# Optimization experiments

Hardware: AMD Instinct MI355X
Metric: run time of the kernel (lower is better)

The kernel has to match this reference:

```python
import jax, jax.numpy as jnp
import numpy as np

B, T, C = 4, 1024, 1024  # batch, tokens, channel (== head `size`)
H = 8                    # num_heads


def setup_inputs() -> dict:
    key = jax.random.key(0)
    kd, kq, kk, kv = jax.random.split(key, 4)
    data = jax.random.normal(kd, (B, T, C), dtype=jnp.float32)
    # torch nn.Linear(size,size,bias=False) weight is [out,in]; one per head, stacked on axis 0
    s = 1.0 / np.sqrt(C)
    Wq = jax.random.uniform(kq, (H, C, C), dtype=jnp.float32, minval=-s, maxval=s)
    Wk = jax.random.uniform(kk, (H, C, C), dtype=jnp.float32, minval=-s, maxval=s)
    Wv = jax.random.uniform(kv, (H, C, C), dtype=jnp.float32, minval=-s, maxval=s)
    return {"data": data, "Wq": Wq, "Wk": Wk, "Wv": Wv}


def reference(data, Wq, Wk, Wv):
    # per-head projections: y = x @ W.T  -> [B,H,T,C]
    q = jnp.einsum('btc,hdc->bhtd', data, Wq)
    k = jnp.einsum('btc,hdc->bhtd', data, Wk)
    v = jnp.einsum('btc,hdc->bhtd', data, Wv)
    scale = 1.0 / jnp.sqrt(jnp.asarray(C, dtype=data.dtype))
    scores = jnp.einsum('bhtd,bhsd->bhts', q, k) * scale  # [B,H,T,T]
    causal = jnp.tril(jnp.ones((T, T), dtype=bool))
    scores = jnp.where(causal, scores, -jnp.inf)
    w = jax.nn.softmax(scores, axis=-1)
    out = jnp.einsum('bhts,bhsd->bhtd', w, v)            # [B,H,T,C]
    # torch.cat over heads on last dim == [B,T,H,C] reshape to [B,T,H*C]
    return out.transpose(0, 2, 1, 3).reshape(B, T, H * C)
```

## Files before the change

### kernel.cpp

```cpp
#include <hip/hip_runtime.h>
#include <hip/hip_fp16.h>


typedef unsigned short u16;
typedef _Float16 f16x8 __attribute__((ext_vector_type(8)));
typedef float f32x4 __attribute__((ext_vector_type(4)));

__device__ __forceinline__ u16 f2h(float f) {
    union { __half h; u16 u; } cv;
    cv.h = __float2half(f);
    return cv.u;
}
__device__ __forceinline__ float h2f(u16 u) {
    union { __half h; u16 u; } cv;
    cv.u = u;
    return __half2float(cv.h);
}

__device__ __forceinline__ void gload_lds16(const u16* g, const u16* lds_base, unsigned off_bytes) {
    unsigned a32 = (unsigned)(uintptr_t)((const char*)lds_base + off_bytes);
    a32 = __builtin_amdgcn_readfirstlane(a32);
    __builtin_amdgcn_global_load_lds(
        (const __attribute__((address_space(1))) void*)(uintptr_t)g,
        (__attribute__((address_space(3))) void*)a32,
        16, 0, 0);
}

#define M_A 0
#define M_B 1
#define M_C 2
#define M_PV 3

template <int MODE>
__global__ __launch_bounds__(512, 2) void mega(
    const u16* __restrict__ dataH, const u16* __restrict__ WvH,
    const u16* __restrict__ WqT, const u16* __restrict__ WkT,
    u16* __restrict__ MTp, u16* __restrict__ Qp, u16* __restrict__ VTa,
    u16* __restrict__ S16, u16* __restrict__ P16,
    float* __restrict__ outF)
{
    const int C = 1024, T = 1024, HC = 8192;
    const int nb = (MODE == M_A ? 192 : MODE == M_B ? 512 :
                    MODE == M_C ? 768 : 256);
    const int chunk = nb >> 3;
    const int phys = blockIdx.x;
    const int o = (phys & 7) * chunk + (phys >> 3);

    __shared__ u16 lds[8 * 8192];

    const int t = threadIdx.x, w = t >> 6, l = t & 63;
    const int wm = w >> 2, wn = w & 3;
    const int frow = l & 15, fch = l >> 4;
    const int clin = w * 64 + l;
    const int srow = clin >> 2;
    const int sch = (clin & 3) ^ ((clin >> 3) & 3);

    const int NPASS = (MODE == M_PV) ? 2 : 1;

    for (int pass = 0; pass < NPASS; ++pass) {
        const u16 *Ab, *Bb;
        int lda, ldb, ldc, NT, tile_m, tile_n;
        float scale = 1.0f;
        u16* out16 = nullptr;
        float* out32 = nullptr;

        int vfill = -1;
        if (MODE == M_A && o >= 128) vfill = o - 128;
        if (MODE == M_C && o >= 320) vfill = o - 320 + 64;

        if (vfill >= 0) {
            const int vz = vfill >> 4, rem = vfill & 15;
            tile_n = rem & 3; tile_m = rem >> 2;
            Ab = WvH + (size_t)(vz & 7) * C * C + (size_t)tile_m * 256 * C;
            Bb = dataH + (size_t)(vz >> 3) * T * C + (size_t)tile_n * 256 * C;
            lda = C; ldb = C; ldc = T;
            out16 = VTa + (size_t)vz * C * T;
            NT = 16;
        } else if (MODE == M_A) {
            const int h = o >> 4, r = o & 15;
            tile_m = r >> 2; tile_n = r & 3;
            Ab = WkT + (size_t)h * C * C + (size_t)tile_m * 256 * C;
            Bb = WqT + (size_t)h * C * C + (size_t)tile_n * 256 * C;
            lda = C; ldb = C; ldc = C;
            out16 = MTp + (size_t)h * C * C;
            NT = 16;
        } else if (MODE == M_B) {
            const int s = o >> 6, ww = o & 63;
            tile_n = (s & 3) * 8 + (ww & 7);
            tile_m = (s >> 2) * 8 + (ww >> 3);
            Ab = dataH + (size_t)tile_m * 256 * C;
            Bb = MTp + (size_t)(tile_n >> 2) * C * C + (size_t)(tile_n & 3) * 256 * C;
            lda = C; ldb = C; ldc = HC;
            out16 = Qp;
            NT = 16;
        } else if (MODE == M_C) {
            const int qz = o / 10, j = o - qz * 10;
            tile_m = (j >= 1) + (j >= 3) + (j >= 6);
            tile_n = j - (tile_m == 0 ? 0 : tile_m == 1 ? 1 : tile_m == 2 ? 3 : 6);
            Ab = Qp + (size_t)(qz >> 3) * T * HC + (size_t)(qz & 7) * C
                    + (size_t)tile_m * 256 * HC;
            Bb = dataH + (size_t)(qz >> 3) * T * C + (size_t)tile_n * 256 * C;
            lda = HC; ldb = C; ldc = T;
            out16 = S16 + (size_t)qz * T * T;
            scale = 1.0f / 32.0f;
            NT = 16;
        } else {
            const int pz = o >> 3, j = o & 7, x = j & 3, hi = j >> 2;
            tile_m = (pass == 0) ? (hi ? 2 : 3) : (hi ? 1 : 0);
            tile_n = x;
            Ab = P16 + (size_t)pz * T * T + (size_t)tile_m * 256 * T;
            Bb = VTa + (size_t)pz * C * T + (size_t)tile_n * 256 * T;
            lda = T; ldb = T; ldc = HC;
            out32 = outF + (size_t)(pz >> 3) * T * HC + (size_t)(pz & 7) * C;
            NT = (tile_m + 1) * 4;
        }

        if (MODE == M_PV) {
            const int pz = o >> 3;
            const int Kend = NT * 64;
            const u16* Sb = S16 + (size_t)pz * T * T + (size_t)tile_m * 256 * T;
            u16* Pb = P16 + (size_t)pz * T * T + (size_t)tile_m * 256 * T;
            for (int rr = w; rr < 256; rr += 8) {
                const int nrow = tile_m * 256 + rr + 1;
                const u16* rp = Sb + (size_t)rr * T;
                float ev[16];
#pragma unroll
                for (int j = 0; j < 4; ++j) {
                    const int col = j * 256 + l * 4;
                    if (col < Kend) {
                        ushort4 v4 = *(const ushort4*)(rp + col);
                        ev[j * 4 + 0] = (col + 0 < nrow) ? h2f(v4.x) : -3.0e38f;
                        ev[j * 4 + 1] = (col + 1 < nrow) ? h2f(v4.y) : -3.0e38f;
                        ev[j * 4 + 2] = (col + 2 < nrow) ? h2f(v4.z) : -3.0e38f;
                        ev[j * 4 + 3] = (col + 3 < nrow) ? h2f(v4.w) : -3.0e38f;
                    } else {
                        ev[j * 4 + 0] = -3.0e38f; ev[j * 4 + 1] = -3.0e38f;
                        ev[j * 4 + 2] = -3.0e38f; ev[j * 4 + 3] = -3.0e38f;
                    }
                }
                float mx = -3.0e38f;
#pragma unroll
                for (int e = 0; e < 16; ++e) mx = fmaxf(mx, ev[e]);
#pragma unroll
                for (int od = 1; od < 64; od <<= 1) mx = fmaxf(mx, __shfl_xor(mx, od));
                float sum = 0.f;
#pragma unroll
                for (int e = 0; e < 16; ++e) { ev[e] = __expf(ev[e] - mx); sum += ev[e]; }
#pragma unroll
                for (int od = 1; od < 64; od <<= 1) sum += __shfl_xor(sum, od);
                const float inv = 1.0f / sum;
#pragma unroll
                for (int j = 0; j < 4; ++j) {
                    const int col = j * 256 + l * 4;
                    if (col < Kend) {
                        ushort4 o4;
                        o4.x = f2h(ev[j * 4 + 0] * inv);
                        o4.y = f2h(ev[j * 4 + 1] * inv);
                        o4.z = f2h(ev[j * 4 + 2] * inv);
                        o4.w = f2h(ev[j * 4 + 3] * inv);
                        *(ushort4*)(Pb + (size_t)rr * T + col) = o4;
                    }
                }
            }
            asm volatile("s_waitcnt vmcnt(0)");
            __builtin_amdgcn_sched_barrier(0);
            __builtin_amdgcn_s_barrier();
        }

        const long eA = (long)srow * lda + sch * 8;
        const long eB = (long)srow * ldb + sch * 8;

        f32x4 acc[8][4] = {};
        f16x8 af[4], bf[4];

#define STAGE(DB, MAT, KS, TT) do {                                            \
        const u16* g_ = (MAT == 0 ? Ab + (size_t)(TT) * 64 + (KS) * 32 + eA    \
                                  : Bb + (size_t)(TT) * 64 + (KS) * 32 + eB);  \
        const u16* hb_ = lds + ((((DB) << 2) | ((MAT) << 1) | (KS)) << 13);    \
        gload_lds16(g_, hb_, (unsigned)(w * 64 * 16));                         \
        gload_lds16(g_ + (size_t)128 * (MAT == 0 ? lda : ldb), hb_,            \
                    (unsigned)((512 + w * 64) * 16));                          \
    } while (0)

#define RD(DB, MAT, KS, ROW)                                                   \
    (*(const f16x8*)((const char*)(lds + ((((DB) << 2) | ((MAT) << 1) | (KS)) << 13)) + \
                     ((unsigned)((ROW) * 64 + fch * 16) ^ ((((ROW) >> 1) & 3) << 4))))

#define VM6 do { asm volatile("s_waitcnt vmcnt(6)"); \
                 __builtin_amdgcn_sched_barrier(0); } while (0)
#define VM0 do { asm volatile("s_waitcnt vmcnt(0)"); \
                 __builtin_amdgcn_sched_barrier(0); } while (0)
#define NOPW ((void)0)

#define PH(DB, KS, MH, WAITC, ...) do {                                        \
        if ((MH) == 0) {                                                       \
            _Pragma("unroll") for (int ni = 0; ni < 4; ++ni)                   \
                bf[ni] = RD(DB, 1, KS, wn * 64 + ni * 16 + frow);              \
        }                                                                      \
        _Pragma("unroll") for (int m4 = 0; m4 < 4; ++m4)                       \
            af[m4] = RD(DB, 0, KS, wm * 128 + ((MH) * 4 + m4) * 16 + frow);    \
        __VA_ARGS__;                                                           \
        __builtin_amdgcn_sched_barrier(0);                                     \
        __builtin_amdgcn_s_barrier();                                          \
        asm volatile("s_waitcnt lgkmcnt(0)");                                  \
        __builtin_amdgcn_sched_barrier(0);                                     \
        __builtin_amdgcn_s_setprio(1);                                         \
        _Pragma("unroll") for (int m4 = 0; m4 < 4; ++m4)                       \
            _Pragma("unroll") for (int ni = 0; ni < 4; ++ni)                   \
                acc[(MH) * 4 + m4][ni] = __builtin_amdgcn_mfma_f32_16x16x32_f16( \
                    af[m4], bf[ni], acc[(MH) * 4 + m4][ni], 0, 0, 0);          \
        __builtin_amdgcn_s_setprio(0);                                         \
        __builtin_amdgcn_sched_barrier(0);                                     \
        WAITC;                                                                 \
        __builtin_amdgcn_s_barrier();                                          \
    } while (0)

        STAGE(0, 1, 0, 0); STAGE(0, 0, 0, 0); STAGE(0, 1, 1, 0); STAGE(0, 0, 1, 0);
        STAGE(1, 1, 0, 1); STAGE(1, 0, 0, 1); STAGE(1, 1, 1, 1);
        VM6;
        __builtin_amdgcn_s_barrier();

        for (int tt = 0; tt < NT; tt += 2) {
            const bool more = (tt + 2) < NT;
            PH(0, 0, 0, NOPW, STAGE(1, 0, 1, tt + 1));
            PH(0, 0, 1, NOPW, if (more) STAGE(0, 1, 0, tt + 2));
            PH(0, 1, 0, NOPW, if (more) STAGE(0, 0, 0, tt + 2));
            PH(0, 1, 1, if (more) VM6; else VM0,
                        if (more) STAGE(0, 1, 1, tt + 2));
            PH(1, 0, 0, NOPW, if (more) STAGE(0, 0, 1, tt + 2));
            PH(1, 0, 1, NOPW, if (more) STAGE(1, 1, 0, tt + 3));
            PH(1, 1, 0, NOPW, if (more) STAGE(1, 0, 0, tt + 3));
            PH(1, 1, 1, if (more) VM6; else VM0,
                        if (more) STAGE(1, 1, 1, tt + 3));
        }
#undef PH
#undef RD
#undef STAGE
#undef VM6
#undef VM0
#undef NOPW

        const int r0 = (l >> 4) * 4, cc = l & 15;
#pragma unroll
        for (int mi = 0; mi < 8; ++mi) {
#pragma unroll
            for (int r = 0; r < 4; ++r) {
                size_t grow = (size_t)(tile_m * 256 + wm * 128 + mi * 16 + r0 + r);
#pragma unroll
                for (int ni = 0; ni < 4; ++ni) {
                    int gcol = tile_n * 256 + wn * 64 + ni * 16 + cc;
                    float v = acc[mi][ni][r] * scale;
                    if (MODE == M_PV)
                        out32[grow * ldc + gcol] = v;
                    else
                        out16[grow * ldc + gcol] = f2h(v);
                }
            }
        }
    }
}

__global__ __launch_bounds__(256) void cast_setup(
    const float* __restrict__ data, const float* __restrict__ Wq,
    const float* __restrict__ Wk, const float* __restrict__ Wv,
    u16* __restrict__ dataH, u16* __restrict__ WqT,
    u16* __restrict__ WkT, u16* __restrict__ WvH)
{
    const int z = blockIdx.z, tx = threadIdx.x, ty = threadIdx.y;
    if (z < 16) {
        const int h = z & 7;
        const float* src = ((z >> 3) ? Wk : Wq) + (size_t)h * 1048576;
        u16* dst = ((z >> 3) ? WkT : WqT) + (size_t)h * 1048576;
        const int r0 = blockIdx.y * 32, c0 = blockIdx.x * 32;
        __shared__ float tile[32][33];
        for (int i = ty; i < 32; i += 8)
            tile[i][tx] = src[(size_t)(r0 + i) * 1024 + c0 + tx];
        __syncthreads();
        for (int i = ty; i < 32; i += 8)
            dst[(size_t)(c0 + i) * 1024 + r0 + tx] = f2h(tile[tx][i]);
    } else {
        const int tid = ty * 32 + tx;
        const int bid = blockIdx.y * 32 + blockIdx.x;
        const int reps = (z == 16) ? 4 : 8;
        const float* src = (z == 16) ? data : Wv;
        u16* dst = (z == 16) ? dataH : WvH;
        for (int k2 = 0; k2 < reps; ++k2) {
            int i = (k2 * 1024 + bid) * 256 + tid;
            float4 v = ((const float4*)src)[i];
            ushort4 o4;
            o4.x = f2h(v.x); o4.y = f2h(v.y); o4.z = f2h(v.z); o4.w = f2h(v.w);
            ((ushort4*)dst)[i] = o4;
        }
    }
}

extern "C" void kernel_launch(void* const* d_in, const int* in_sizes, int n_in,
                              void* d_out, int out_size, void* d_ws, size_t ws_size,
                              hipStream_t stream)
{
    (void)in_sizes; (void)n_in; (void)out_size; (void)ws_size;
    const int B = 4, T = 1024, C = 1024, H = 8;
    const int BT = B * T, HC = H * C;

    const float* data = (const float*)d_in[0];
    const float* Wq = (const float*)d_in[1];
    const float* Wk = (const float*)d_in[2];
    const float* Wv = (const float*)d_in[3];
    float* out = (float*)d_out;

    char* p = (char*)d_ws;
    const size_t nData = (size_t)BT * C;
    const size_t nW = (size_t)H * C * C;
    const size_t nAll = (size_t)BT * HC;
    const size_t nS = (size_t)B * H * T * T;
    u16* dataH = (u16*)p; p += nData * 2;
    u16* WvH = (u16*)p; p += nW * 2;
    u16* WqT = (u16*)p; p += nW * 2;
    u16* WkT = (u16*)p; p += nW * 2;
    u16* MTp = (u16*)p; p += nW * 2;
    u16* Qp = (u16*)p; p += nAll * 2;
    u16* VTa = (u16*)p; p += nAll * 2;
    u16* S16 = (u16*)p; p += nS * 2;
    u16* P16 = (u16*)p; p += nS * 2;

    cast_setup<<<dim3(32, 32, 18), dim3(32, 8), 0, stream>>>(
        data, Wq, Wk, Wv, dataH, WqT, WkT, WvH);

    mega<M_A><<<dim3(192), dim3(512), 0, stream>>>(
        dataH, WvH, WqT, WkT, MTp, Qp, VTa, S16, P16, out);

    mega<M_B><<<dim3(512), dim3(512), 0, stream>>>(
        dataH, WvH, WqT, WkT, MTp, Qp, VTa, S16, P16, out);

    mega<M_C><<<dim3(768), dim3(512), 0, stream>>>(
        dataH, WvH, WqT, WkT, MTp, Qp, VTa, S16, P16, out);

    mega<M_PV><<<dim3(256), dim3(512), 0, stream>>>(
        dataH, WvH, WqT, WkT, MTp, Qp, VTa, S16, P16, out);
}
```

Before: 450.5 us.

## Fuse four GEMM phase launches into one persistent kernel with grid barriers

Replaces the four separate mega kernel launches with a single persistent 256-block kernel. The phases are separated by software grid barriers built on atomic counters, which are reset inside the setup kernel. Work is redistributed per phase: the projection, score and V tiles are looped over blocks, and the softmax becomes a row-parallel pass over all rows instead of running inside each PV block. The goal is to remove launch gaps and kernel tail effects. The costs are spin-wait barriers and a reliance on all 256 blocks being co-resident (two per CU), otherwise the kernel deadlocks.

Result: slower. 588.8 us (median of 3 runs) (+30.7%).

```diff
diff --git a/kernel.cpp b/kernel.cpp
--- a/kernel.cpp
+++ b/kernel.cpp
@@ -26,152 +26,36 @@
         16, 0, 0);
 }
 
-#define M_A 0
-#define M_B 1
-#define M_C 2
-#define M_PV 3
-
-template <int MODE>
-__global__ __launch_bounds__(512, 2) void mega(
-    const u16* __restrict__ dataH, const u16* __restrict__ WvH,
-    const u16* __restrict__ WqT, const u16* __restrict__ WkT,
-    u16* __restrict__ MTp, u16* __restrict__ Qp, u16* __restrict__ VTa,
-    u16* __restrict__ S16, u16* __restrict__ P16,
-    float* __restrict__ outF)
+__device__ __forceinline__ void gridbar(unsigned* bar, int idx) {
+    __syncthreads();
+    if (threadIdx.x == 0) {
+        __threadfence();
+        unsigned* c = bar + idx * 32;
+        __hip_atomic_fetch_add(c, 1u, __ATOMIC_ACQ_REL, __HIP_MEMORY_SCOPE_AGENT);
+        while (__hip_atomic_load(c, __ATOMIC_ACQUIRE, __HIP_MEMORY_SCOPE_AGENT) < 256u) {
+            __builtin_amdgcn_s_sleep(2);
+        }
+        __threadfence();
+    }
+    __syncthreads();
+}
+
+template <int F32OUT>
+__device__ __forceinline__ void gemm_tile(
+    const u16* __restrict__ Ab, const u16* __restrict__ Bb,
+    int lda, int ldb, int NT, float scale, void* outp, int ldc, u16* lds)
 {
-    const int C = 1024, T = 1024, HC = 8192;
-    const int nb = (MODE == M_A ? 192 : MODE == M_B ? 512 :
-                    MODE == M_C ? 768 : 256);
-    const int chunk = nb >> 3;
-    const int phys = blockIdx.x;
-    const int o = (phys & 7) * chunk + (phys >> 3);
-
-    __shared__ u16 lds[8 * 8192];
-
     const int t = threadIdx.x, w = t >> 6, l = t & 63;
     const int wm = w >> 2, wn = w & 3;
     const int frow = l & 15, fch = l >> 4;
     const int clin = w * 64 + l;
     const int srow = clin >> 2;
     const int sch = (clin & 3) ^ ((clin >> 3) & 3);
-
-    const int NPASS = (MODE == M_PV) ? 2 : 1;
-
-    for (int pass = 0; pass < NPASS; ++pass) {
-        const u16 *Ab, *Bb;
-        int lda, ldb, ldc, NT, tile_m, tile_n;
-        float scale = 1.0f;
-        u16* out16 = nullptr;
-        float* out32 = nullptr;
-
-        int vfill = -1;
-        if (MODE == M_A && o >= 128) vfill = o - 128;
-        if (MODE == M_C && o >= 320) vfill = o - 320 + 64;
-
-        if (vfill >= 0) {
-            const int vz = vfill >> 4, rem = vfill & 15;
-            tile_n = rem & 3; tile_m = rem >> 2;
-            Ab = WvH + (size_t)(vz & 7) * C * C + (size_t)tile_m * 256 * C;
-            Bb = dataH + (size_t)(vz >> 3) * T * C + (size_t)tile_n * 256 * C;
-            lda = C; ldb = C; ldc = T;
-            out16 = VTa + (size_t)vz * C * T;
-            NT = 16;
-        } else if (MODE == M_A) {
-            const int h = o >> 4, r = o & 15;
-            tile_m = r >> 2; tile_n = r & 3;
-            Ab = WkT + (size_t)h * C * C + (size_t)tile_m * 256 * C;
-            Bb = WqT + (size_t)h * C * C + (size_t)tile_n * 256 * C;
-            lda = C; ldb = C; ldc = C;
-            out16 = MTp + (size_t)h * C * C;
-            NT = 16;
-        } else if (MODE == M_B) {
-            const int s = o >> 6, ww = o & 63;
-            tile_n = (s & 3) * 8 + (ww & 7);
-            tile_m = (s >> 2) * 8 + (ww >> 3);
-            Ab = dataH + (size_t)tile_m * 256 * C;
-            Bb = MTp + (size_t)(tile_n >> 2) * C * C + (size_t)(tile_n & 3) * 256 * C;
-            lda = C; ldb = C; ldc = HC;
-            out16 = Qp;
-            NT = 16;
-        } else if (MODE == M_C) {
-            const int qz = o / 10, j = o - qz * 10;
-            tile_m = (j >= 1) + (j >= 3) + (j >= 6);
-            tile_n = j - (tile_m == 0 ? 0 : tile_m == 1 ? 1 : tile_m == 2 ? 3 : 6);
-            Ab = Qp + (size_t)(qz >> 3) * T * HC + (size_t)(qz & 7) * C
-                    + (size_t)tile_m * 256 * HC;
-            Bb = dataH + (size_t)(qz >> 3) * T * C + (size_t)tile_n * 256 * C;
-            lda = HC; ldb = C; ldc = T;
-            out16 = S16 + (size_t)qz * T * T;
-            scale = 1.0f / 32.0f;
-            NT = 16;
-        } else {
-            const int pz = o >> 3, j = o & 7, x = j & 3, hi = j >> 2;
-            tile_m = (pass == 0) ? (hi ? 2 : 3) : (hi ? 1 : 0);
-            tile_n = x;
-            Ab = P16 + (size_t)pz * T * T + (size_t)tile_m * 256 * T;
-            Bb = VTa + (size_t)pz * C * T + (size_t)tile_n * 256 * T;
-            lda = T; ldb = T; ldc = HC;
-            out32 = outF + (size_t)(pz >> 3) * T * HC + (size_t)(pz & 7) * C;
-            NT = (tile_m + 1) * 4;
-        }
-
-        if (MODE == M_PV) {
-            const int pz = o >> 3;
-            const int Kend = NT * 64;
-            const u16* Sb = S16 + (size_t)pz * T * T + (size_t)tile_m * 256 * T;
-            u16* Pb = P16 + (size_t)pz * T * T + (size_t)tile_m * 256 * T;
-            for (int rr = w; rr < 256; rr += 8) {
-                const int nrow = tile_m * 256 + rr + 1;
-                const u16* rp = Sb + (size_t)rr * T;
-                float ev[16];
-#pragma unroll
-                for (int j = 0; j < 4; ++j) {
-                    const int col = j * 256 + l * 4;
-                    if (col < Kend) {
-                        ushort4 v4 = *(const ushort4*)(rp + col);
-                        ev[j * 4 + 0] = (col + 0 < nrow) ? h2f(v4.x) : -3.0e38f;
-                        ev[j * 4 + 1] = (col + 1 < nrow) ? h2f(v4.y) : -3.0e38f;
-                        ev[j * 4 + 2] = (col + 2 < nrow) ? h2f(v4.z) : -3.0e38f;
-                        ev[j * 4 + 3] = (col + 3 < nrow) ? h2f(v4.w) : -3.0e38f;
-                    } else {
-                        ev[j * 4 + 0] = -3.0e38f; ev[j * 4 + 1] = -3.0e38f;
-                        ev[j * 4 + 2] = -3.0e38f; ev[j * 4 + 3] = -3.0e38f;
-                    }
-                }
-                float mx = -3.0e38f;
-#pragma unroll
-                for (int e = 0; e < 16; ++e) mx = fmaxf(mx, ev[e]);
-#pragma unroll
-                for (int od = 1; od < 64; od <<= 1) mx = fmaxf(mx, __shfl_xor(mx, od));
-                float sum = 0.f;
-#pragma unroll
-                for (int e = 0; e < 16; ++e) { ev[e] = __expf(ev[e] - mx); sum += ev[e]; }
-#pragma unroll
-                for (int od = 1; od < 64; od <<= 1) sum += __shfl_xor(sum, od);
-                const float inv = 1.0f / sum;
-#pragma unroll
-                for (int j = 0; j < 4; ++j) {
-                    const int col = j * 256 + l * 4;
-                    if (col < Kend) {
-                        ushort4 o4;
-                        o4.x = f2h(ev[j * 4 + 0] * inv);
-                        o4.y = f2h(ev[j * 4 + 1] * inv);
-                        o4.z = f2h(ev[j * 4 + 2] * inv);
-                        o4.w = f2h(ev[j * 4 + 3] * inv);
-                        *(ushort4*)(Pb + (size_t)rr * T + col) = o4;
-                    }
-                }
-            }
-            asm volatile("s_waitcnt vmcnt(0)");
-            __builtin_amdgcn_sched_barrier(0);
-            __builtin_amdgcn_s_barrier();
-        }
-
-        const long eA = (long)srow * lda + sch * 8;
-        const long eB = (long)srow * ldb + sch * 8;
-
-        f32x4 acc[8][4] = {};
-        f16x8 af[4], bf[4];
+    const long eA = (long)srow * lda + sch * 8;
+    const long eB = (long)srow * ldb + sch * 8;
+
+    f32x4 acc[8][4] = {};
+    f16x8 af[4], bf[4];
 
 #define STAGE(DB, MAT, KS, TT) do {                                            \
         const u16* g_ = (MAT == 0 ? Ab + (size_t)(TT) * 64 + (KS) * 32 + eA    \
@@ -215,24 +99,24 @@
         __builtin_amdgcn_s_barrier();                                          \
     } while (0)
 
-        STAGE(0, 1, 0, 0); STAGE(0, 0, 0, 0); STAGE(0, 1, 1, 0); STAGE(0, 0, 1, 0);
-        STAGE(1, 1, 0, 1); STAGE(1, 0, 0, 1); STAGE(1, 1, 1, 1);
-        VM6;
-        __builtin_amdgcn_s_barrier();
-
-        for (int tt = 0; tt < NT; tt += 2) {
-            const bool more = (tt + 2) < NT;
-            PH(0, 0, 0, NOPW, STAGE(1, 0, 1, tt + 1));
-            PH(0, 0, 1, NOPW, if (more) STAGE(0, 1, 0, tt + 2));
-            PH(0, 1, 0, NOPW, if (more) STAGE(0, 0, 0, tt + 2));
-            PH(0, 1, 1, if (more) VM6; else VM0,
-                        if (more) STAGE(0, 1, 1, tt + 2));
-            PH(1, 0, 0, NOPW, if (more) STAGE(0, 0, 1, tt + 2));
-            PH(1, 0, 1, NOPW, if (more) STAGE(1, 1, 0, tt + 3));
-            PH(1, 1, 0, NOPW, if (more) STAGE(1, 0, 0, tt + 3));
-            PH(1, 1, 1, if (more) VM6; else VM0,
-                        if (more) STAGE(1, 1, 1, tt + 3));
-        }
+    STAGE(0, 1, 0, 0); STAGE(0, 0, 0, 0); STAGE(0, 1, 1, 0); STAGE(0, 0, 1, 0);
+    STAGE(1, 1, 0, 1); STAGE(1, 0, 0, 1); STAGE(1, 1, 1, 1);
+    VM6;
+    __builtin_amdgcn_s_barrier();
+
+    for (int tt = 0; tt < NT; tt += 2) {
+        const bool more = (tt + 2) < NT;
+        PH(0, 0, 0, NOPW, STAGE(1, 0, 1, tt + 1));
+        PH(0, 0, 1, NOPW, if (more) STAGE(0, 1, 0, tt + 2));
+        PH(0, 1, 0, NOPW, if (more) STAGE(0, 0, 0, tt + 2));
+        PH(0, 1, 1, if (more) VM6; else VM0,
+                    if (more) STAGE(0, 1, 1, tt + 2));
+        PH(1, 0, 0, NOPW, if (more) STAGE(0, 0, 1, tt + 2));
+        PH(1, 0, 1, NOPW, if (more) STAGE(1, 1, 0, tt + 3));
+        PH(1, 1, 0, NOPW, if (more) STAGE(1, 0, 0, tt + 3));
+        PH(1, 1, 1, if (more) VM6; else VM0,
+                    if (more) STAGE(1, 1, 1, tt + 3));
+    }
 #undef PH
 #undef RD
 #undef STAGE
@@ -240,23 +124,153 @@
 #undef VM0
 #undef NOPW
 
-        const int r0 = (l >> 4) * 4, cc = l & 15;
-#pragma unroll
-        for (int mi = 0; mi < 8; ++mi) {
-#pragma unroll
-            for (int r = 0; r < 4; ++r) {
-                size_t grow = (size_t)(tile_m * 256 + wm * 128 + mi * 16 + r0 + r);
-#pragma unroll
-                for (int ni = 0; ni < 4; ++ni) {
-                    int gcol = tile_n * 256 + wn * 64 + ni * 16 + cc;
-                    float v = acc[mi][ni][r] * scale;
-                    if (MODE == M_PV)
-                        out32[grow * ldc + gcol] = v;
-                    else
-                        out16[grow * ldc + gcol] = f2h(v);
+    const int r0 = (l >> 4) * 4, cc = l & 15;
+#pragma unroll
+    for (int mi = 0; mi < 8; ++mi) {
+#pragma unroll
+        for (int r = 0; r < 4; ++r) {
+            size_t roff = (size_t)(wm * 128 + mi * 16 + r0 + r) * ldc;
+#pragma unroll
+            for (int ni = 0; ni < 4; ++ni) {
+                int gcol = wn * 64 + ni * 16 + cc;
+                float v = acc[mi][ni][r] * scale;
+                if (F32OUT)
+                    ((float*)outp)[roff + gcol] = v;
+                else
+                    ((u16*)outp)[roff + gcol] = f2h(v);
+            }
+        }
+    }
+}
+
+__global__ __launch_bounds__(512, 2) void fused(
+    const u16* __restrict__ dataH, const u16* __restrict__ WvH,
+    const u16* __restrict__ WqT, const u16* __restrict__ WkT,
+    u16* __restrict__ MTp, u16* __restrict__ Qp, u16* __restrict__ VTa,
+    u16* __restrict__ S16, u16* __restrict__ P16,
+    float* __restrict__ outF, unsigned* __restrict__ bar)
+{
+    const int C = 1024, T = 1024, HC = 8192;
+    __shared__ u16 lds[8 * 8192];
+    const int phys = blockIdx.x;
+    const int o = (phys & 7) * 32 + (phys >> 3);
+
+    {
+        const u16 *Ab, *Bb; u16* op; int ldc2;
+        if (o < 128) {
+            const int h = o >> 4, r2 = o & 15, tm = r2 >> 2, tn = r2 & 3;
+            Ab = WkT + (size_t)h * C * C + (size_t)tm * 256 * C;
+            Bb = WqT + (size_t)h * C * C + (size_t)tn * 256 * C;
+            op = MTp + (size_t)h * C * C + (size_t)tm * 256 * C + tn * 256;
+            ldc2 = C;
+        } else {
+            const int v = o - 128, vz = v >> 4, rem = v & 15;
+            const int tn = rem & 3, tm = rem >> 2;
+            Ab = WvH + (size_t)(vz & 7) * C * C + (size_t)tm * 256 * C;
+            Bb = dataH + (size_t)(vz >> 3) * T * C + (size_t)tn * 256 * C;
+            op = VTa + (size_t)vz * C * T + (size_t)tm * 256 * T + tn * 256;
+            ldc2 = T;
+        }
+        gemm_tile<0>(Ab, Bb, C, C, 16, 1.0f, op, ldc2, lds);
+    }
+    gridbar(bar, 0);
+
+    for (int i = 0; i < 2; ++i) {
+        const int u = o + (i << 8);
+        const int s = u >> 6, ww = u & 63;
+        const int tn = (s & 3) * 8 + (ww & 7);
+        const int tm = (s >> 2) * 8 + (ww >> 3);
+        const u16* Ab = dataH + (size_t)tm * 256 * C;
+        const u16* Bb = MTp + (size_t)(tn >> 2) * C * C + (size_t)(tn & 3) * 256 * C;
+        u16* op = Qp + (size_t)tm * 256 * HC + tn * 256;
+        gemm_tile<0>(Ab, Bb, C, C, 16, 1.0f, op, HC, lds);
+    }
+    gridbar(bar, 1);
+
+    for (int i = 0; i < 3; ++i) {
+        const int u = o + (i << 8);
+        if (u >= 704) break;
+        const u16 *Ab, *Bb; u16* op; int lda2, ldc2; float sc;
+        if (u < 320) {
+            const int qz = u / 10, j = u - qz * 10;
+            const int tm = (j >= 1) + (j >= 3) + (j >= 6);
+            const int tn = j - (tm == 0 ? 0 : tm == 1 ? 1 : tm == 2 ? 3 : 6);
+            Ab = Qp + (size_t)(qz >> 3) * T * HC + (size_t)(qz & 7) * C
+                    + (size_t)tm * 256 * HC;
+            Bb = dataH + (size_t)(qz >> 3) * T * C + (size_t)tn * 256 * C;
+            op = S16 + (size_t)qz * T * T + (size_t)tm * 256 * T + tn * 256;
+            lda2 = HC; ldc2 = T; sc = 1.0f / 32.0f;
+        } else {
+            const int v = u - 320 + 128, vz = v >> 4, rem = v & 15;
+            const int tn = rem & 3, tm = rem >> 2;
+            Ab = WvH + (size_t)(vz & 7) * C * C + (size_t)tm * 256 * C;
+            Bb = dataH + (size_t)(vz >> 3) * T * C + (size_t)tn * 256 * C;
+            op = VTa + (size_t)vz * C * T + (size_t)tm * 256 * T + tn * 256;
+            lda2 = C; ldc2 = T; sc = 1.0f;
+        }
+        gemm_tile<0>(Ab, Bb, lda2, C, 16, sc, op, ldc2, lds);
+    }
+    gridbar(bar, 2);
+
+    {
+        const int w = threadIdx.x >> 6, l = threadIdx.x & 63;
+        for (int i = w; i < 128; i += 8) {
+            const int rid = o + (i << 8);
+            const int z = rid >> 10, tq = rid & 1023;
+            const u16* rp = S16 + ((size_t)z * T + tq) * T;
+            u16* pp = P16 + ((size_t)z * T + tq) * T;
+            const int nvalid = tq + 1;
+            const int nseg = (tq >> 8) + 1;
+            float ev[16];
+#pragma unroll
+            for (int j = 0; j < 4; ++j) {
+                const int col = j * 256 + l * 4;
+                if (j < nseg) {
+                    ushort4 v4 = *(const ushort4*)(rp + col);
+                    ev[j * 4 + 0] = (col + 0 < nvalid) ? h2f(v4.x) : -3.0e38f;
+                    ev[j * 4 + 1] = (col + 1 < nvalid) ? h2f(v4.y) : -3.0e38f;
+                    ev[j * 4 + 2] = (col + 2 < nvalid) ? h2f(v4.z) : -3.0e38f;
+                    ev[j * 4 + 3] = (col + 3 < nvalid) ? h2f(v4.w) : -3.0e38f;
+                } else {
+                    ev[j * 4 + 0] = -3.0e38f; ev[j * 4 + 1] = -3.0e38f;
+                    ev[j * 4 + 2] = -3.0e38f; ev[j * 4 + 3] = -3.0e38f;
                 }
             }
-        }
+            float mx = -3.0e38f;
+#pragma unroll
+            for (int e = 0; e < 16; ++e) mx = fmaxf(mx, ev[e]);
+#pragma unroll
+            for (int od = 1; od < 64; od <<= 1) mx = fmaxf(mx, __shfl_xor(mx, od));
+            float sum = 0.f;
+#pragma unroll
+            for (int e = 0; e < 16; ++e) { ev[e] = __expf(ev[e] - mx); sum += ev[e]; }
+#pragma unroll
+            for (int od = 1; od < 64; od <<= 1) sum += __shfl_xor(sum, od);
+            const float inv = 1.0f / sum;
+#pragma unroll
+            for (int j = 0; j < 4; ++j) {
+                const int col = j * 256 + l * 4;
+                if (j < nseg) {
+                    ushort4 o4;
+                    o4.x = f2h(ev[j * 4 + 0] * inv);
+                    o4.y = f2h(ev[j * 4 + 1] * inv);
+                    o4.z = f2h(ev[j * 4 + 2] * inv);
+                    o4.w = f2h(ev[j * 4 + 3] * inv);
+                    *(ushort4*)(pp + col) = o4;
+                }
+            }
+        }
+    }
+    gridbar(bar, 3);
+
+    for (int pass = 0; pass < 2; ++pass) {
+        const int pz = o >> 3, j = o & 7, x = j & 3, hi = j >> 2;
+        const int tm = (pass == 0) ? (hi ? 2 : 3) : (hi ? 1 : 0);
+        const u16* Ab = P16 + (size_t)pz * T * T + (size_t)tm * 256 * T;
+        const u16* Bb = VTa + (size_t)pz * C * T + (size_t)x * 256 * T;
+        float* op = outF + (size_t)(pz >> 3) * T * HC + (size_t)(pz & 7) * C
+                         + (size_t)tm * 256 * HC + x * 256;
+        gemm_tile<1>(Ab, Bb, T, T, (tm + 1) * 4, 1.0f, op, HC, lds);
     }
 }
 
@@ -264,9 +278,12 @@
     const float* __restrict__ data, const float* __restrict__ Wq,
     const float* __restrict__ Wk, const float* __restrict__ Wv,
     u16* __restrict__ dataH, u16* __restrict__ WqT,
-    u16* __restrict__ WkT, u16* __restrict__ WvH)
+    u16* __restrict__ WkT, u16* __restrict__ WvH, unsigned* __restrict__ bar)
 {
     const int z = blockIdx.z, tx = threadIdx.x, ty = threadIdx.y;
+    if (z == 17 && blockIdx.x == 0 && blockIdx.y == 0 && tx == 0 && ty == 0) {
+        bar[0] = 0; bar[32] = 0; bar[64] = 0; bar[96] = 0;
+    }
     if (z < 16) {
         const int h = z & 7;
         const float* src = ((z >> 3) ? Wk : Wq) + (size_t)h * 1048576;
@@ -322,19 +339,11 @@
     u16* VTa = (u16*)p; p += nAll * 2;
     u16* S16 = (u16*)p; p += nS * 2;
     u16* P16 = (u16*)p; p += nS * 2;
+    unsigned* bar = (unsigned*)(((uintptr_t)p + 255) & ~(uintptr_t)255);
 
     cast_setup<<<dim3(32, 32, 18), dim3(32, 8), 0, stream>>>(
-        data, Wq, Wk, Wv, dataH, WqT, WkT, WvH);
-
-    mega<M_A><<<dim3(192), dim3(512), 0, stream>>>(
-        dataH, WvH, WqT, WkT, MTp, Qp, VTa, S16, P16, out);
-
-    mega<M_B><<<dim3(512), dim3(512), 0, stream>>>(
-        dataH, WvH, WqT, WkT, MTp, Qp, VTa, S16, P16, out);
-
-    mega<M_C><<<dim3(768), dim3(512), 0, stream>>>(
-        dataH, WvH, WqT, WkT, MTp, Qp, VTa, S16, P16, out);
-
-    mega<M_PV><<<dim3(256), dim3(512), 0, stream>>>(
-        dataH, WvH, WqT, WkT, MTp, Qp, VTa, S16, P16, out);
-}
+        data, Wq, Wk, Wv, dataH, WqT, WkT, WvH, bar);
+
+    fused<<<dim3(256), dim3(512), 0, stream>>>(
+        dataH, WvH, WqT, WkT, MTp, Qp, VTa, S16, P16, out, bar);
+}
```
